# Kernel optimization log

Hardware: AMD Instinct MI355X
Metric: run time of the kernel (lower is better)

## Reference

```python
import jax, jax.numpy as jnp
import numpy as np

N_NODES = 10000
N_EDGES = 160000
F_IN, D, DEPTH, F_OUT = 6, 512, 10, 1


def setup_inputs() -> dict:
    key = jax.random.key(0)
    ks = jax.random.split(key, 10)
    features = jax.random.normal(ks[0], (N_NODES, F_IN), dtype=jnp.float32)
    src = jax.random.randint(ks[1], (N_EDGES,), 0, N_NODES, dtype=jnp.int32)
    dst = jax.random.randint(ks[2], (N_EDGES,), 0, N_NODES, dtype=jnp.int32)
    s_in = 1.0 / np.sqrt(F_IN)
    s_h = 1.0 / np.sqrt(D)
    W_in = jax.random.uniform(ks[3], (F_IN, D), jnp.float32, -s_in, s_in)
    b_in = jax.random.uniform(ks[4], (D,), jnp.float32, -s_in, s_in)
    Ws = jax.random.uniform(ks[5], (DEPTH, D, D), jnp.float32, -s_h, s_h)
    bs = jax.random.uniform(ks[6], (DEPTH, D), jnp.float32, -s_h, s_h)
    W_out = jax.random.uniform(ks[7], (D, F_OUT), jnp.float32, -s_h, s_h)
    b_out = jax.random.uniform(ks[8], (F_OUT,), jnp.float32, -s_h, s_h)
    return {"features": features, "W_in": W_in, "b_in": b_in, "Ws": Ws,
            "bs": bs, "W_out": W_out, "b_out": b_out, "src": src, "dst": dst}


def reference(features, W_in, b_in, Ws, bs, W_out, b_out, src, dst):
    n = features.shape[0]
    # GCNLayer: aggregate = scatter-sum of neighbor features (copy_src + sum), then Linear
    agg = jax.ops.segment_sum(features[src], dst, num_segments=n)  # [N, F_in]
    x = jax.nn.relu(agg @ W_in + b_in)  # ReLU only after input layer (per forward)

    def step(x, wb):
        W, b = wb
        a = jax.ops.segment_sum(x[src], dst, num_segments=n)  # [N, D]
        return a @ W + b, None  # no activation between hidden GCN layers

    x, _ = jax.lax.scan(step, x, (Ws, bs))
    return x @ W_out + b_out  # [N, 1]
```

## Files before the change

### kernel.cpp

```cpp
#include <hip/hip_runtime.h>


#define N_NODES 10000
#define N_EDGES 160000
#define DEPTH   10

#define NB_G 40
#define NB_C 33
#define NB   (NB_G + NB_C)
#define BT   1024
#define NTHG (NB_G * BT)
#define NPB  250
#define ECAP 8192

typedef unsigned long long u64;

__device__ __forceinline__ int ldAi(const int* p) {
    return __hip_atomic_load(p, __ATOMIC_RELAXED, __HIP_MEMORY_SCOPE_AGENT);
}
__device__ __forceinline__ void stAi(int* p, int v) {
    __hip_atomic_store(p, v, __ATOMIC_RELAXED, __HIP_MEMORY_SCOPE_AGENT);
}
__device__ __forceinline__ float ldAf(const float* p) {
    return __hip_atomic_load(p, __ATOMIC_RELAXED, __HIP_MEMORY_SCOPE_AGENT);
}
__device__ __forceinline__ void stAf(float* p, float v) {
    __hip_atomic_store(p, v, __ATOMIC_RELAXED, __HIP_MEMORY_SCOPE_AGENT);
}
__device__ __forceinline__ u64 ld8(const u64* p) {
    return __hip_atomic_load(p, __ATOMIC_RELAXED, __HIP_MEMORY_SCOPE_AGENT);
}
__device__ __forceinline__ void st8(u64* p, u64 v) {
    __hip_atomic_store(p, v, __ATOMIC_RELAXED, __HIP_MEMORY_SCOPE_AGENT);
}
__device__ __forceinline__ u64 packf(float f) {
    union { float f; unsigned u; } c; c.f = f;
    return (1ull << 32) | (u64)c.u;
}
__device__ __forceinline__ float unpackf(u64 v) {
    union { unsigned u; float f; } c; c.u = (unsigned)v;
    return c.f;
}
#define READY(v) ((unsigned)((v) >> 32) != 0u)

__device__ __forceinline__ float pollf(const u64* p) {
    u64 v = ld8(p);
    while (!READY(v)) { __builtin_amdgcn_s_sleep(1); v = ld8(p); }
    return unpackf(v);
}

__device__ __forceinline__ void group_bar(int* flags, int gi, int n, int target) {
    const int tx = threadIdx.x;
    asm volatile("s_waitcnt vmcnt(0)" ::: "memory");
    __syncthreads();
    if (tx == 0) stAi(&flags[gi * 32], target);
    if (tx < n && tx != gi) {
        while (ldAi(&flags[tx * 32]) < target) __builtin_amdgcn_s_sleep(1);
    }
    __syncthreads();
}

extern "C" __global__ void __launch_bounds__(BT, 1) gcn_mega(
    const float* __restrict__ features, const float* __restrict__ W_in,
    const float* __restrict__ b_in, const float* __restrict__ Ws,
    const float* __restrict__ bs, const float* __restrict__ W_out,
    const float* __restrict__ b_out, const int* __restrict__ src,
    const int* __restrict__ dst, float* __restrict__ out,
    int* g_arrive, int* deg_done, int* scan_done, u64* gamma8, u64* vslab,
    int* deg, u64* esrc8, float* rb0, float* rb1, int* row_ptr, int* cursor)
{
    __shared__ int   lds_e[ECAP];
    __shared__ float s_Wb[4096];
    __shared__ float s_vt[512];
    __shared__ float s_gam[16];
    __shared__ int   s_info[2];
    __shared__ int   s_wsum[16];

    const int tx = threadIdx.x;
    const int bx = blockIdx.x;

    if (bx >= NB_G) {
        const int gi   = bx - NB_G;
        const int cw   = gi * 16 + (tx >> 6);
        const int lane = tx & 63;
        if (cw > 512) return;
        for (int s = 0; s < DEPTH; s++) {
            const int l = 9 - s;
            const float* rowp = (cw < 512)
                ? (Ws + (size_t)l * (512 * 512) + (size_t)cw * 512)
                : (bs + (size_t)l * 512);
            float wrow[8];
#pragma unroll
            for (int c = 0; c < 8; c++) wrow[c] = rowp[lane + 64 * c];
            float vin[8];
            if (s == 0) {
#pragma unroll
                for (int c = 0; c < 8; c++) vin[c] = W_out[lane + 64 * c];
            } else {
                const u64* vb = vslab + (size_t)s * 512;
                u64 raw[8];
#pragma unroll
                for (int c = 0; c < 8; c++) raw[c] = ld8(vb + lane + 64 * c);
                for (;;) {
                    bool ok = true;
#pragma unroll
                    for (int c = 0; c < 8; c++)
                        if (!READY(raw[c])) { ok = false; raw[c] = ld8(vb + lane + 64 * c); }
                    if (ok) break;
                    __builtin_amdgcn_s_sleep(1);
                }
#pragma unroll
                for (int c = 0; c < 8; c++) vin[c] = unpackf(raw[c]);
            }
            float acc = 0.f;
#pragma unroll
            for (int c = 0; c < 8; c++) acc += wrow[c] * vin[c];
#pragma unroll
            for (int off = 32; off; off >>= 1) acc += __shfl_xor(acc, off, 64);
            if (lane == 0) {
                if (cw < 512) st8(vslab + (size_t)(s + 1) * 512 + cw, packf(acc));
                else          st8(gamma8 + l, packf(acc));
            }
        }
        return;
    }


    {
        const int t0 = bx * BT + tx;
        for (int e = t0; e < N_EDGES; e += NTHG) atomicAdd(&deg[dst[e]], 1);
    }
    for (int idx = tx; idx < 4096; idx += BT) {
        int j = idx >> 3, k = idx & 7;
        float v = 0.f;
        if (k < 6) v = W_in[k * 512 + j];
        else if (k == 6) v = b_in[j];
        s_Wb[idx] = v;
    }
    asm volatile("s_waitcnt vmcnt(0)" ::: "memory");
    __syncthreads();
    if (tx == 0) stAi(&deg_done[bx * 32], 1);

    if (bx == 0) {
        if (tx < NB_G) {
            while (ldAi(&deg_done[tx * 32]) < 1) __builtin_amdgcn_s_sleep(1);
        }
        __syncthreads();
        const int lane = tx & 63, wid = tx >> 6;
        const bool sact = tx < 1000;
        int lv[10];
        int ssum = 0;
        if (sact) {
#pragma unroll
            for (int i = 0; i < 10; i++) { lv[i] = ldAi(&deg[tx * 10 + i]); ssum += lv[i]; }
        }
        int v = ssum;
#pragma unroll
        for (int off = 1; off < 64; off <<= 1) {
            int u = __shfl_up(v, off, 64);
            if (lane >= off) v += u;
        }
        if (lane == 63) s_wsum[wid] = v;
        __syncthreads();
        if (wid == 0) {
            int w = (lane < 16) ? s_wsum[lane] : 0;
#pragma unroll
            for (int off = 1; off < 16; off <<= 1) {
                int u = __shfl_up(w, off, 64);
                if (lane >= off) w += u;
            }
            if (lane < 16) s_wsum[lane] = w;
        }
        __syncthreads();
        if (sact) {
            int run = (wid ? s_wsum[wid - 1] : 0) + (v - ssum);
#pragma unroll
            for (int i = 0; i < 10; i++) {
                stAi(&row_ptr[tx * 10 + i], run);
                stAi(&cursor[tx * 10 + i], run);
                run += lv[i];
            }
            if (tx == 999) stAi(&row_ptr[N_NODES], run);
        }
        asm volatile("s_waitcnt vmcnt(0)" ::: "memory");
        __syncthreads();
        if (tx == 0) stAi(scan_done, 1);
    } else {
        if (tx == 0) {
            while (ldAi(scan_done) < 1) __builtin_amdgcn_s_sleep(1);
        }
        __syncthreads();
    }

    {
        const int t0 = bx * BT + tx;
        for (int e = t0; e < N_EDGES; e += NTHG) {
            int d = dst[e];
            unsigned sv = (unsigned)src[e];
            int pos = atomicAdd(&cursor[d], 1);
            st8(&esrc8[pos], (1ull << 32) | (u64)sv);
        }
    }

    if (tx == 0) {
        s_info[0] = ldAi(&row_ptr[bx * NPB]);
        s_info[1] = ldAi(&row_ptr[bx * NPB + NPB]);
    }
    __syncthreads();
    const int e_lo = s_info[0];
    const int slen = s_info[1] - e_lo;
    const bool use_lds = (slen <= ECAP);
    if (use_lds) {
        for (int i = tx; i < slen; i += BT) {
            u64 v = ld8(&esrc8[e_lo + i]);
            while (!READY(v)) { __builtin_amdgcn_s_sleep(1); v = ld8(&esrc8[e_lo + i]); }
            lds_e[i] = (int)(unsigned)v;
        }
    }
    __syncthreads();

    const int node = bx * NPB + (tx >> 2);
    const int sub  = tx & 3;
    const bool act = tx < 4 * NPB;
    int ns = 0, ne = 0;
    float a0 = 0.f, a1 = 0.f, a2 = 0.f, a3 = 0.f, a4 = 0.f, a5 = 0.f;
    if (act) {
        ns = ldAi(&row_ptr[node]);
        ne = ldAi(&row_ptr[node + 1]);
        for (int pp = ns + sub; pp < ne; pp += 4) {
            int j;
            if (use_lds) j = lds_e[pp - e_lo];
            else {
                u64 v = ld8(&esrc8[pp]);
                while (!READY(v)) { __builtin_amdgcn_s_sleep(1); v = ld8(&esrc8[pp]); }
                j = (int)(unsigned)v;
            }
            const float2* f = (const float2*)(features + (size_t)j * 6);
            float2 f0 = f[0], f1 = f[1], f2 = f[2];
            a0 += f0.x; a1 += f0.y; a2 += f1.x;
            a3 += f1.y; a4 += f2.x; a5 += f2.y;
        }
        a0 += __shfl_xor(a0, 1, 64); a0 += __shfl_xor(a0, 2, 64);
        a1 += __shfl_xor(a1, 1, 64); a1 += __shfl_xor(a1, 2, 64);
        a2 += __shfl_xor(a2, 1, 64); a2 += __shfl_xor(a2, 2, 64);
        a3 += __shfl_xor(a3, 1, 64); a3 += __shfl_xor(a3, 2, 64);
        a4 += __shfl_xor(a4, 1, 64); a4 += __shfl_xor(a4, 2, 64);
        a5 += __shfl_xor(a5, 1, 64); a5 += __shfl_xor(a5, 2, 64);
    }

    if (tx < 512) s_vt[tx] = pollf(vslab + 10 * 512 + tx);
    else if (tx < 512 + DEPTH) s_gam[tx - 512] = pollf(gamma8 + (tx - 512));
    __syncthreads();

    if (act) {
        const float4* Wb4 = (const float4*)s_Wb;
        float zacc = 0.f;
#pragma unroll 4
        for (int jj = 0; jj < 128; jj++) {
            int j = (jj << 2) | sub;
            float4 wA = Wb4[2 * j];
            float4 wB = Wb4[2 * j + 1];
            float tv = wB.z + a0 * wA.x + a1 * wA.y + a2 * wA.z +
                       a3 * wA.w + a4 * wB.x + a5 * wB.y;
            zacc += fmaxf(tv, 0.f) * s_vt[j];
        }
        zacc += __shfl_xor(zacc, 1, 64);
        zacc += __shfl_xor(zacc, 2, 64);
        if (sub == 0) stAf(&rb0[node], zacc);
    }
    int gt = 1;
    group_bar(g_arrive, bx, NB_G, gt++);

    for (int l = 0; l < DEPTH; l++) {
        if (act) {
            const float* rin = (l & 1) ? rb1 : rb0;
            float h0 = 0.f, h1 = 0.f, h2 = 0.f, h3 = 0.f;
            int pp = ns + sub;
            if (use_lds) {
                for (; pp + 12 < ne; pp += 16) {
                    h0 += ldAf(&rin[lds_e[pp - e_lo]]);
                    h1 += ldAf(&rin[lds_e[pp + 4 - e_lo]]);
                    h2 += ldAf(&rin[lds_e[pp + 8 - e_lo]]);
                    h3 += ldAf(&rin[lds_e[pp + 12 - e_lo]]);
                }
                for (; pp < ne; pp += 4) h0 += ldAf(&rin[lds_e[pp - e_lo]]);
            } else {
                for (; pp < ne; pp += 4) {
                    u64 ev = ld8(&esrc8[pp]);
                    while (!READY(ev)) { __builtin_amdgcn_s_sleep(1); ev = ld8(&esrc8[pp]); }
                    h0 += ldAf(&rin[(int)(unsigned)ev]);
                }
            }
            float hs = (h0 + h1) + (h2 + h3);
            hs += __shfl_xor(hs, 1, 64);
            hs += __shfl_xor(hs, 2, 64);
            if (sub == 0) {
                float res = hs + s_gam[l];
                if (l == DEPTH - 1) out[node] = res + b_out[0];
                else stAf(&((l & 1) ? rb0 : rb1)[node], res);
            }
        }
        if (l < DEPTH - 1) group_bar(g_arrive, bx, NB_G, gt++);
    }
}


extern "C" void kernel_launch(void* const* d_in, const int* in_sizes, int n_in,
                              void* d_out, int out_size, void* d_ws, size_t ws_size,
                              hipStream_t stream) {
    const float* features = (const float*)d_in[0];
    const float* W_in     = (const float*)d_in[1];
    const float* b_in     = (const float*)d_in[2];
    const float* Ws       = (const float*)d_in[3];
    const float* bs       = (const float*)d_in[4];
    const float* W_out    = (const float*)d_in[5];
    const float* b_out    = (const float*)d_in[6];
    const int*   src      = (const int*)d_in[7];
    const int*   dst      = (const int*)d_in[8];
    float* out = (float*)d_out;

    char* base = (char*)d_ws;
    int* g_arrive  = (int*)(base + 0);
    int* deg_done  = (int*)(base + 5120);
    int* scan_done = (int*)(base + 10240);
    u64* gamma8    = (u64*)(base + 10368);
    u64* vslab     = (u64*)(base + 10496);
    int* deg       = (int*)(base + 55552);
    u64* esrc8     = (u64*)(base + 95616);
    float* rb0     = (float*)(base + 1375616);
    float* rb1     = (float*)(base + 1415680);
    const size_t MEMSET_END = 1455744;
    int* row_ptr   = (int*)(base + 1455744);
    int* cursor    = (int*)(base + 1495808);

    hipMemsetAsync(base, 0, MEMSET_END, stream);

    gcn_mega<<<NB, BT, 0, stream>>>(features, W_in, b_in, Ws, bs, W_out, b_out,
                                    src, dst, out,
                                    g_arrive, deg_done, scan_done, gamma8,
                                    vslab, deg, esrc8, rb0, rb1,
                                    row_ptr, cursor);
}
```

Measured before the change: 206.0 us.

## Replace per-entry ready-flag polling with group barriers and shrink memset

The per-edge 64-bit ready-tagged CSR entries are replaced by plain 32-bit indices. The point-to-point degree and scan flags and the per-element readiness spins give way to full group barriers after the degree count, the prefix scan and the CSR fill. This drops the 1.3MB esrc memset and halves CSR storage and load width. The cost is an extra grid-wide barrier that removes the overlap between CSR fill and consumption.

```diff
diff --git a/kernel.cpp b/kernel.cpp
--- a/kernel.cpp
+++ b/kernel.cpp
@@ -66,8 +66,8 @@
     const float* __restrict__ bs, const float* __restrict__ W_out,
     const float* __restrict__ b_out, const int* __restrict__ src,
     const int* __restrict__ dst, float* __restrict__ out,
-    int* g_arrive, int* deg_done, int* scan_done, u64* gamma8, u64* vslab,
-    int* deg, u64* esrc8, float* rb0, float* rb1, int* row_ptr, int* cursor)
+    int* g_arrive, u64* gamma8, u64* vslab, int* deg, int* esrc,
+    float* rb0, float* rb1, int* row_ptr, int* cursor)
 {
     __shared__ int   lds_e[ECAP];
     __shared__ float s_Wb[4096];
@@ -125,6 +125,8 @@
         return;
     }
 
+    const int gi = bx;
+    int gt = 1;
 
     {
         const int t0 = bx * BT + tx;
@@ -137,15 +139,9 @@
         else if (k == 6) v = b_in[j];
         s_Wb[idx] = v;
     }
-    asm volatile("s_waitcnt vmcnt(0)" ::: "memory");
-    __syncthreads();
-    if (tx == 0) stAi(&deg_done[bx * 32], 1);
+    group_bar(g_arrive, gi, NB_G, gt++);
 
     if (bx == 0) {
-        if (tx < NB_G) {
-            while (ldAi(&deg_done[tx * 32]) < 1) __builtin_amdgcn_s_sleep(1);
-        }
-        __syncthreads();
         const int lane = tx & 63, wid = tx >> 6;
         const bool sact = tx < 1000;
         int lv[10];
@@ -182,25 +178,19 @@
             }
             if (tx == 999) stAi(&row_ptr[N_NODES], run);
         }
-        asm volatile("s_waitcnt vmcnt(0)" ::: "memory");
-        __syncthreads();
-        if (tx == 0) stAi(scan_done, 1);
-    } else {
-        if (tx == 0) {
-            while (ldAi(scan_done) < 1) __builtin_amdgcn_s_sleep(1);
-        }
-        __syncthreads();
-    }
+    }
+    group_bar(g_arrive, gi, NB_G, gt++);
 
     {
         const int t0 = bx * BT + tx;
         for (int e = t0; e < N_EDGES; e += NTHG) {
             int d = dst[e];
-            unsigned sv = (unsigned)src[e];
+            int sv = src[e];
             int pos = atomicAdd(&cursor[d], 1);
-            st8(&esrc8[pos], (1ull << 32) | (u64)sv);
-        }
-    }
+            stAi(&esrc[pos], sv);
+        }
+    }
+    group_bar(g_arrive, gi, NB_G, gt++);
 
     if (tx == 0) {
         s_info[0] = ldAi(&row_ptr[bx * NPB]);
@@ -211,11 +201,7 @@
     const int slen = s_info[1] - e_lo;
     const bool use_lds = (slen <= ECAP);
     if (use_lds) {
-        for (int i = tx; i < slen; i += BT) {
-            u64 v = ld8(&esrc8[e_lo + i]);
-            while (!READY(v)) { __builtin_amdgcn_s_sleep(1); v = ld8(&esrc8[e_lo + i]); }
-            lds_e[i] = (int)(unsigned)v;
-        }
+        for (int i = tx; i < slen; i += BT) lds_e[i] = ldAi(&esrc[e_lo + i]);
     }
     __syncthreads();
 
@@ -230,11 +216,7 @@
         for (int pp = ns + sub; pp < ne; pp += 4) {
             int j;
             if (use_lds) j = lds_e[pp - e_lo];
-            else {
-                u64 v = ld8(&esrc8[pp]);
-                while (!READY(v)) { __builtin_amdgcn_s_sleep(1); v = ld8(&esrc8[pp]); }
-                j = (int)(unsigned)v;
-            }
+            else         j = ldAi(&esrc[pp]);
             const float2* f = (const float2*)(features + (size_t)j * 6);
             float2 f0 = f[0], f1 = f[1], f2 = f[2];
             a0 += f0.x; a1 += f0.y; a2 += f1.x;
@@ -268,8 +250,7 @@
         zacc += __shfl_xor(zacc, 2, 64);
         if (sub == 0) stAf(&rb0[node], zacc);
     }
-    int gt = 1;
-    group_bar(g_arrive, bx, NB_G, gt++);
+    group_bar(g_arrive, gi, NB_G, gt++);
 
     for (int l = 0; l < DEPTH; l++) {
         if (act) {
@@ -285,11 +266,7 @@
                 }
                 for (; pp < ne; pp += 4) h0 += ldAf(&rin[lds_e[pp - e_lo]]);
             } else {
-                for (; pp < ne; pp += 4) {
-                    u64 ev = ld8(&esrc8[pp]);
-                    while (!READY(ev)) { __builtin_amdgcn_s_sleep(1); ev = ld8(&esrc8[pp]); }
-                    h0 += ldAf(&rin[(int)(unsigned)ev]);
-                }
+                for (; pp < ne; pp += 4) h0 += ldAf(&rin[ldAi(&esrc[pp])]);
             }
             float hs = (h0 + h1) + (h2 + h3);
             hs += __shfl_xor(hs, 1, 64);
@@ -300,7 +277,7 @@
                 else stAf(&((l & 1) ? rb0 : rb1)[node], res);
             }
         }
-        if (l < DEPTH - 1) group_bar(g_arrive, bx, NB_G, gt++);
+        if (l < DEPTH - 1) group_bar(g_arrive, gi, NB_G, gt++);
     }
 }
 
@@ -320,24 +297,21 @@
     float* out = (float*)d_out;
 
     char* base = (char*)d_ws;
-    int* g_arrive  = (int*)(base + 0);
-    int* deg_done  = (int*)(base + 5120);
-    int* scan_done = (int*)(base + 10240);
-    u64* gamma8    = (u64*)(base + 10368);
-    u64* vslab     = (u64*)(base + 10496);
-    int* deg       = (int*)(base + 55552);
-    u64* esrc8     = (u64*)(base + 95616);
-    float* rb0     = (float*)(base + 1375616);
-    float* rb1     = (float*)(base + 1415680);
-    const size_t MEMSET_END = 1455744;
-    int* row_ptr   = (int*)(base + 1455744);
-    int* cursor    = (int*)(base + 1495808);
+    int*   g_arrive = (int*)(base + 0);
+    u64*   gamma8   = (u64*)(base + 5120);
+    u64*   vslab    = (u64*)(base + 5248);
+    int*   deg      = (int*)(base + 50304);
+    float* rb0      = (float*)(base + 90368);
+    float* rb1      = (float*)(base + 130432);
+    const size_t MEMSET_END = 170496;
+    int* esrc       = (int*)(base + 170496);
+    int* row_ptr    = (int*)(base + 810496);
+    int* cursor     = (int*)(base + 850560);
 
     hipMemsetAsync(base, 0, MEMSET_END, stream);
 
     gcn_mega<<<NB, BT, 0, stream>>>(features, W_in, b_in, Ws, bs, W_out, b_out,
                                     src, dst, out,
-                                    g_arrive, deg_done, scan_done, gamma8,
-                                    vslab, deg, esrc8, rb0, rb1,
-                                    row_ptr, cursor);
-}
+                                    g_arrive, gamma8, vslab, deg, esrc,
+                                    rb0, rb1, row_ptr, cursor);
+}
```

Result: no change. 205.1 us (-0.4%).
